# Optimization experiments

Hardware: AMD Instinct MI355X
Metric: run time of the kernel (lower is better)

The kernel has to match this reference:

```python
import jax, jax.numpy as jnp
import numpy as np

D_MODEL = 1024
NUM_HEADS = 16
NUM_KV_HEADS = 4
HEAD_DIM = D_MODEL // NUM_HEADS  # 64
THETA = 10000.0
MAX_SEQ_LEN = 4096


def _rope_tables(max_seq_len, d_k, theta):
    k_vec = jnp.arange(0, d_k, 2, dtype=jnp.float32) / d_k
    freq = 1.0 / (theta ** k_vec)                       # (d_k/2,)
    ang = jnp.arange(max_seq_len, dtype=jnp.float32)[:, None] * freq[None, :]
    return jnp.cos(ang), jnp.sin(ang)                   # each (max_seq_len, d_k/2)


def _apply_rope(x, pos, cos_table, sin_table):
    # x: (b, h, l, d), pos: (b, l)
    cos = cos_table[pos][:, None, :, :]                 # (b, 1, l, d/2)
    sin = sin_table[pos][:, None, :, :]
    even, odd = x[..., 0::2], x[..., 1::2]
    r1 = even * cos - odd * sin
    r2 = even * sin + odd * cos
    return jnp.stack([r1, r2], axis=-1).reshape(x.shape)  # interleave back


def setup_inputs() -> dict:
    key = jax.random.key(0)
    ks = jax.random.split(key, 6)
    B, L, D = 1, 4096, D_MODEL
    std = (2.0 / (D + D)) ** 0.5
    std_kv = (2.0 / (D + HEAD_DIM * NUM_KV_HEADS)) ** 0.5
    x = jax.random.normal(ks[0], (B, L, D), dtype=jnp.float32)
    Wq = jax.random.normal(ks[1], (D, D), dtype=jnp.float32) * std
    Wk = jax.random.normal(ks[2], (HEAD_DIM * NUM_KV_HEADS, D), dtype=jnp.float32) * std_kv
    Wv = jax.random.normal(ks[3], (HEAD_DIM * NUM_KV_HEADS, D), dtype=jnp.float32) * std_kv
    Wo = jax.random.normal(ks[4], (D, D), dtype=jnp.float32) * std
    token_positions = jnp.broadcast_to(jnp.arange(L, dtype=jnp.int32), (B, L))
    return {"x": x, "Wq": Wq, "Wk": Wk, "Wv": Wv, "Wo": Wo,
            "token_positions": token_positions}


def reference(x, Wq, Wk, Wv, Wo, token_positions):
    B, L, D = x.shape
    H, Hkv, Dh = NUM_HEADS, NUM_KV_HEADS, HEAD_DIM
    n_rep = H // Hkv
    cos_t, sin_t = _rope_tables(MAX_SEQ_LEN, Dh, THETA)

    q = (x @ Wq.T).reshape(B, L, H, Dh).transpose(0, 2, 1, 3)      # b h l d
    k = (x @ Wk.T).reshape(B, L, Hkv, Dh).transpose(0, 2, 1, 3)    # b g l d
    v = (x @ Wv.T).reshape(B, L, Hkv, Dh).transpose(0, 2, 1, 3)

    q = _apply_rope(q, token_positions, cos_t, sin_t)
    k = _apply_rope(k, token_positions, cos_t, sin_t)

    # GQA: group query heads by kv head
    qg = q.reshape(B, Hkv, n_rep, L, Dh)
    scores = jnp.einsum('bgrqd,bgkd->bgrqk', qg, k) / jnp.sqrt(jnp.float32(Dh))
    causal = jnp.tril(jnp.ones((L, L), dtype=bool))
    scores = jnp.where(causal, scores, -jnp.inf)
    weights = jax.nn.softmax(scores, axis=-1)
    out = jnp.einsum('bgrqk,bgkd->bgrqd', weights, v)              # b g r q d
    out = out.reshape(B, H, L, Dh).transpose(0, 2, 1, 3).reshape(B, L, D)
    return out @ Wo.T
```

## Files before the change

kernel.cpp:

```cpp
#include <hip/hip_runtime.h>
#include <hip/hip_bf16.h>
#include <math.h>

typedef __bf16 bf16;
typedef __bf16 v8bf __attribute__((ext_vector_type(8)));
typedef __bf16 v4bf __attribute__((ext_vector_type(4)));
typedef __bf16 v2bf __attribute__((ext_vector_type(2)));
typedef float f32x4 __attribute__((ext_vector_type(4)));
typedef float f32x16 __attribute__((ext_vector_type(16)));

#define L_SEQ 4096
#define DMODEL 1024
#define NHEADS 16
#define DH 64
#define NEG_BIG (-1e30f)
#define LN1E4_64 0.14391156f
#define SCL2 0.18033688f

static __device__ __forceinline__ unsigned pkbf(float x, float y) {
    v2bf t; t[0] = (bf16)x; t[1] = (bf16)y;
    return __builtin_bit_cast(unsigned, t);
}

__global__ void convert_all(const float* __restrict__ x, const float* __restrict__ wq,
                            const float* __restrict__ wk, const float* __restrict__ wv,
                            const float* __restrict__ wo,
                            bf16* __restrict__ xb, bf16* __restrict__ wqkvb,
                            bf16* __restrict__ wob) {
    int i = (blockIdx.x * 256 + threadIdx.x) * 4;
    const float* src;
    bf16* dst;
    if (i < 4194304)      { src = x  + i;             dst = xb    + i; }
    else if (i < 5242880) { src = wq + (i - 4194304); dst = wqkvb + (i - 4194304); }
    else if (i < 5505024) { src = wk + (i - 5242880); dst = wqkvb + 1048576 + (i - 5242880); }
    else if (i < 5767168) { src = wv + (i - 5505024); dst = wqkvb + 1310720 + (i - 5505024); }
    else                  { src = wo + (i - 5767168); dst = wob   + (i - 5767168); }
    f32x4 v = *(const f32x4*)src;
    v4bf r;
#pragma unroll
    for (int j = 0; j < 4; j++) r[j] = (bf16)v[j];
    *(v4bf*)dst = r;
}

__global__ __launch_bounds__(512) void gemm_qkv(const bf16* __restrict__ A,
                                                const bf16* __restrict__ W,
                                                bf16* __restrict__ Qb,
                                                bf16* __restrict__ Kb,
                                                bf16* __restrict__ Vtg,
                                                const int* __restrict__ tp) {
    __shared__ bf16 As[128][68];
    __shared__ bf16 Bs[128][68];
    const int K = 1024;
    const int tid = threadIdx.x;
    const int w = tid >> 6, lane = tid & 63;
    const int quad = lane >> 4, l16 = lane & 15;
    const int wm = (w & 1) * 64, wn = (w >> 1) * 32;
    const int bm = blockIdx.y * 128, bn = blockIdx.x * 128;

    f32x4 acc[4][2];
#pragma unroll
    for (int mf = 0; mf < 4; mf++)
#pragma unroll
        for (int nf = 0; nf < 2; nf++) acc[mf][nf] = (f32x4){0.f, 0.f, 0.f, 0.f};

    const int sr = tid >> 2;
    const int scb = (tid & 3) * 16;

    v8bf pa0, pa1, pb0, pb1;
    {
        const bf16* ap = &A[(size_t)(bm + sr) * K + scb];
        const bf16* bp = &W[(size_t)(bn + sr) * K + scb];
        pa0 = *(const v8bf*)ap; pa1 = *(const v8bf*)(ap + 8);
        pb0 = *(const v8bf*)bp; pb1 = *(const v8bf*)(bp + 8);
        *(v8bf*)&As[sr][scb] = pa0; *(v8bf*)&As[sr][scb + 8] = pa1;
        *(v8bf*)&Bs[sr][scb] = pb0; *(v8bf*)&Bs[sr][scb + 8] = pb1;
    }

    for (int kt = 0; kt < K; kt += 64) {
        __syncthreads();
        const bool more = (kt + 64) < K;
        if (more) {
            const bf16* ap = &A[(size_t)(bm + sr) * K + kt + 64 + scb];
            const bf16* bp = &W[(size_t)(bn + sr) * K + kt + 64 + scb];
            pa0 = *(const v8bf*)ap; pa1 = *(const v8bf*)(ap + 8);
            pb0 = *(const v8bf*)bp; pb1 = *(const v8bf*)(bp + 8);
        }
#pragma unroll
        for (int kf = 0; kf < 2; kf++) {
            v8bf a[4], b[2];
#pragma unroll
            for (int mf = 0; mf < 4; mf++) a[mf] = *(v8bf*)&As[wm + mf * 16 + l16][kf * 32 + quad * 8];
#pragma unroll
            for (int nf = 0; nf < 2; nf++) b[nf] = *(v8bf*)&Bs[wn + nf * 16 + l16][kf * 32 + quad * 8];
#pragma unroll
            for (int mf = 0; mf < 4; mf++)
#pragma unroll
                for (int nf = 0; nf < 2; nf++)
                    acc[mf][nf] = __builtin_amdgcn_mfma_f32_16x16x32_bf16(a[mf], b[nf], acc[mf][nf], 0, 0, 0);
        }
        __syncthreads();
        if (more) {
            *(v8bf*)&As[sr][scb] = pa0; *(v8bf*)&As[sr][scb + 8] = pa1;
            *(v8bf*)&Bs[sr][scb] = pb0; *(v8bf*)&Bs[sr][scb + 8] = pb1;
        }
    }

    if (bn < 1024) {
#pragma unroll
        for (int mf = 0; mf < 4; mf++) {
            int pos_[4];
#pragma unroll
            for (int r = 0; r < 4; r++) pos_[r] = tp[bm + wm + mf * 16 + quad * 4 + r];
#pragma unroll
            for (int nf = 0; nf < 2; nf++) {
                const int col = bn + wn + nf * 16 + l16;
                float fr = __expf(-(float)((col & 63) & ~1) * LN1E4_64);
#pragma unroll
                for (int r = 0; r < 4; r++) {
                    float v = acc[mf][nf][r];
                    float sn, cs;
                    __sincosf((float)pos_[r] * fr, &sn, &cs);
                    float p = __shfl_xor(v, 1);
                    float res = (l16 & 1) ? (p * sn + v * cs) : (v * cs - p * sn);
                    int row = bm + wm + mf * 16 + quad * 4 + r;
                    Qb[(size_t)row * DMODEL + col] = (bf16)res;
                }
            }
        }
    } else if (bn < 1280) {
#pragma unroll
        for (int mf = 0; mf < 4; mf++) {
            int pos_[4];
#pragma unroll
            for (int r = 0; r < 4; r++) pos_[r] = tp[bm + wm + mf * 16 + quad * 4 + r];
#pragma unroll
            for (int nf = 0; nf < 2; nf++) {
                const int kcol = bn - 1024 + wn + nf * 16 + l16;
                float fr = __expf(-(float)((kcol & 63) & ~1) * LN1E4_64);
#pragma unroll
                for (int r = 0; r < 4; r++) {
                    float v = acc[mf][nf][r];
                    float sn, cs;
                    __sincosf((float)pos_[r] * fr, &sn, &cs);
                    float p = __shfl_xor(v, 1);
                    float res = (l16 & 1) ? (p * sn + v * cs) : (v * cs - p * sn);
                    int row = bm + wm + mf * 16 + quad * 4 + r;
                    Kb[(size_t)row * 256 + kcol] = (bf16)res;
                }
            }
        }
    } else {
#pragma unroll
        for (int mf = 0; mf < 4; mf++)
#pragma unroll
            for (int nf = 0; nf < 2; nf++) {
                v4bf pk;
#pragma unroll
                for (int r = 0; r < 4; r++) pk[r] = (bf16)acc[mf][nf][r];
                int vcol = bn - 1280 + wn + nf * 16 + l16;
                int row = bm + wm + mf * 16 + quad * 4;
                *(v4bf*)&Vtg[(size_t)vcol * L_SEQ + row] = pk;
            }
    }
}

__global__ __launch_bounds__(512) void gemm_out(const bf16* __restrict__ A,
                                                const bf16* __restrict__ W,
                                                float* __restrict__ C) {
    __shared__ bf16 As[128][68];
    __shared__ bf16 Bs[128][68];
    const int K = 1024, N = 1024;
    const int tid = threadIdx.x;
    const int w = tid >> 6, lane = tid & 63;
    const int quad = lane >> 4, l16 = lane & 15;
    const int wm = (w & 1) * 64, wn = (w >> 1) * 32;
    const int bm = blockIdx.y * 128, bn = blockIdx.x * 128;

    f32x4 acc[4][2];
#pragma unroll
    for (int mf = 0; mf < 4; mf++)
#pragma unroll
        for (int nf = 0; nf < 2; nf++) acc[mf][nf] = (f32x4){0.f, 0.f, 0.f, 0.f};

    const int sr = tid >> 2;
    const int scb = (tid & 3) * 16;

    v8bf pa0, pa1, pb0, pb1;
    {
        const bf16* ap = &A[(size_t)(bm + sr) * K + scb];
        const bf16* bp = &W[(size_t)(bn + sr) * K + scb];
        pa0 = *(const v8bf*)ap; pa1 = *(const v8bf*)(ap + 8);
        pb0 = *(const v8bf*)bp; pb1 = *(const v8bf*)(bp + 8);
        *(v8bf*)&As[sr][scb] = pa0; *(v8bf*)&As[sr][scb + 8] = pa1;
        *(v8bf*)&Bs[sr][scb] = pb0; *(v8bf*)&Bs[sr][scb + 8] = pb1;
    }

    for (int kt = 0; kt < K; kt += 64) {
        __syncthreads();
        const bool more = (kt + 64) < K;
        if (more) {
            const bf16* ap = &A[(size_t)(bm + sr) * K + kt + 64 + scb];
            const bf16* bp = &W[(size_t)(bn + sr) * K + kt + 64 + scb];
            pa0 = *(const v8bf*)ap; pa1 = *(const v8bf*)(ap + 8);
            pb0 = *(const v8bf*)bp; pb1 = *(const v8bf*)(bp + 8);
        }
#pragma unroll
        for (int kf = 0; kf < 2; kf++) {
            v8bf a[4], b[2];
#pragma unroll
            for (int mf = 0; mf < 4; mf++) a[mf] = *(v8bf*)&As[wm + mf * 16 + l16][kf * 32 + quad * 8];
#pragma unroll
            for (int nf = 0; nf < 2; nf++) b[nf] = *(v8bf*)&Bs[wn + nf * 16 + l16][kf * 32 + quad * 8];
#pragma unroll
            for (int mf = 0; mf < 4; mf++)
#pragma unroll
                for (int nf = 0; nf < 2; nf++)
                    acc[mf][nf] = __builtin_amdgcn_mfma_f32_16x16x32_bf16(a[mf], b[nf], acc[mf][nf], 0, 0, 0);
        }
        __syncthreads();
        if (more) {
            *(v8bf*)&As[sr][scb] = pa0; *(v8bf*)&As[sr][scb + 8] = pa1;
            *(v8bf*)&Bs[sr][scb] = pb0; *(v8bf*)&Bs[sr][scb + 8] = pb1;
        }
    }
#pragma unroll
    for (int mf = 0; mf < 4; mf++)
#pragma unroll
        for (int nf = 0; nf < 2; nf++)
#pragma unroll
            for (int r = 0; r < 4; r++) {
                int row = bm + wm + mf * 16 + quad * 4 + r;
                int col = bn + wn + nf * 16 + l16;
                C[(size_t)row * N + col] = acc[mf][nf][r];
            }
}

__global__ __launch_bounds__(256, 2) void flash7(const bf16* __restrict__ Q,
                                                 const bf16* __restrict__ Kb,
                                                 const bf16* __restrict__ Vtg,
                                                 bf16* __restrict__ O0,
                                                 bf16* __restrict__ O1,
                                                 float* __restrict__ ML) {
    __shared__ bf16 Ks[128][68];
    __shared__ bf16 Vt[64][132];
    const int h = blockIdx.y, kvh = h >> 2;
    const int bx = blockIdx.x;
    const int tid = threadIdx.x;
    const int w = tid >> 6, lane = tid & 63;
    const int l32 = lane & 31, hi = lane >> 5;
    const int krow = tid >> 1, kcb = (tid & 1) * 32;
    const int vr = tid >> 2, vcb = (tid & 3) * 32;

    for (int p = 0; p < 2; p++) {
        const int qb = p ? (31 - bx) : bx;
        const int T = qb + 1;
        const int k0 = p ? ((T + 1) >> 1) : 0;
        const int k1 = p ? T : ((T + 1) >> 1);
        bf16* Op = p ? O1 : O0;
        float* mlp = ML + (size_t)(p * NHEADS + h) * L_SEQ * 2;

        if (k0 >= k1) {
            for (int i = tid; i < 128 * 64; i += 256) {
                int rr = i >> 6, cc = i & 63;
                Op[(size_t)(qb * 128 + rr) * DMODEL + h * DH + cc] = (bf16)0.f;
            }
            if (tid < 128) {
                mlp[(qb * 128 + tid) * 2 + 0] = NEG_BIG;
                mlp[(qb * 128 + tid) * 2 + 1] = 0.f;
            }
            continue;
        }

        const int qrow = qb * 128 + w * 32 + l32;
        v8bf qf[4];
#pragma unroll
        for (int d16 = 0; d16 < 4; d16++)
            qf[d16] = *(const v8bf*)&Q[(size_t)qrow * DMODEL + h * DH + d16 * 16 + hi * 8];

        f32x16 oaccT[2];
#pragma unroll
        for (int d = 0; d < 2; d++)
#pragma unroll
            for (int r = 0; r < 16; r++) oaccT[d][r] = 0.f;
        float m_i = NEG_BIG, l_i = 0.f;

        v8bf kreg[4], vreg[4];
        {
            const bf16* ks = &Kb[(size_t)(k0 * 128 + krow) * 256 + kvh * DH + kcb];
            const bf16* vs = &Vtg[(size_t)(kvh * DH + vr) * L_SEQ + k0 * 128 + vcb];
#pragma unroll
            for (int u = 0; u < 4; u++) { kreg[u] = *(const v8bf*)&ks[8 * u]; vreg[u] = *(const v8bf*)&vs[8 * u]; }
            __syncthreads();
#pragma unroll
            for (int u = 0; u < 4; u++) { *(v8bf*)&Ks[krow][kcb + 8 * u] = kreg[u]; *(v8bf*)&Vt[vr][vcb + 8 * u] = vreg[u]; }
        }

        for (int kb = k0; kb < k1; kb++) {
            __syncthreads();
            if (kb + 1 < k1) {
                const bf16* ks = &Kb[(size_t)((kb + 1) * 128 + krow) * 256 + kvh * DH + kcb];
                const bf16* vs = &Vtg[(size_t)(kvh * DH + vr) * L_SEQ + (kb + 1) * 128 + vcb];
#pragma unroll
                for (int u = 0; u < 4; u++) { kreg[u] = *(const v8bf*)&ks[8 * u]; vreg[u] = *(const v8bf*)&vs[8 * u]; }
            }

            f32x16 s[4];
            __builtin_amdgcn_s_setprio(1);
#pragma unroll
            for (int n = 0; n < 4; n++) {
#pragma unroll
                for (int r = 0; r < 16; r++) s[n][r] = 0.f;
#pragma unroll
                for (int d16 = 0; d16 < 4; d16++) {
                    v8bf av = *(v8bf*)&Ks[n * 32 + l32][d16 * 16 + hi * 8];
                    s[n] = __builtin_amdgcn_mfma_f32_32x32x16_bf16(av, qf[d16], s[n], 0, 0, 0);
                }
            }
            __builtin_amdgcn_s_setprio(0);

            if (kb == qb) {
#pragma unroll
                for (int n = 0; n < 4; n++) {
                    int kbase = kb * 128 + n * 32 + 4 * hi;
#pragma unroll
                    for (int r = 0; r < 16; r++) {
                        int key = kbase + (r & 3) + 8 * (r >> 2);
                        s[n][r] = (key <= qrow) ? s[n][r] * SCL2 : NEG_BIG;
                    }
                }
            } else {
#pragma unroll
                for (int n = 0; n < 4; n++)
#pragma unroll
                    for (int r = 0; r < 16; r++) s[n][r] *= SCL2;
            }

            float mx = s[0][0];
#pragma unroll
            for (int n = 0; n < 4; n++)
#pragma unroll
                for (int r = 0; r < 16; r++) mx = fmaxf(mx, s[n][r]);
            mx = fmaxf(mx, __shfl_xor(mx, 32));

            float mnew = fmaxf(m_i, mx);
            float alpha = exp2f(m_i - mnew);
            float rs = 0.f;
#pragma unroll
            for (int n = 0; n < 4; n++)
#pragma unroll
                for (int r = 0; r < 16; r++) {
                    float pv = exp2f(s[n][r] - mnew);
                    s[n][r] = pv;
                    rs += pv;
                }
            rs += __shfl_xor(rs, 32);
            l_i = l_i * alpha + rs;
            m_i = mnew;
#pragma unroll
            for (int d = 0; d < 2; d++)
#pragma unroll
                for (int r = 0; r < 16; r++) oaccT[d][r] *= alpha;

            __builtin_amdgcn_s_setprio(1);
#pragma unroll
            for (int n = 0; n < 4; n++) {
#pragma unroll
                for (int u = 0; u < 2; u++) {
                    const int ro = u * 8;
                    unsigned a0 = pkbf(s[n][ro + 0], s[n][ro + 1]);
                    unsigned a1 = pkbf(s[n][ro + 2], s[n][ro + 3]);
                    unsigned b0 = pkbf(s[n][ro + 4], s[n][ro + 5]);
                    unsigned b1 = pkbf(s[n][ro + 6], s[n][ro + 7]);
#if __has_builtin(__builtin_amdgcn_permlane32_swap)
                    auto s0 = __builtin_amdgcn_permlane32_swap(a0, b0, false, false);
                    auto s1 = __builtin_amdgcn_permlane32_swap(a1, b1, false, false);
                    unsigned w0 = s0[0], w2 = s0[1], w1 = s1[0], w3 = s1[1];
#else
                    unsigned t0 = hi ? a0 : b0;
                    unsigned r0 = __shfl_xor(t0, 32);
                    unsigned w0 = hi ? r0 : a0, w2 = hi ? b0 : r0;
                    unsigned t1 = hi ? a1 : b1;
                    unsigned r1 = __shfl_xor(t1, 32);
                    unsigned w1 = hi ? r1 : a1, w3 = hi ? b1 : r1;
#endif
                    union { unsigned uu[4]; v8bf v; } pf;
                    pf.uu[0] = w0; pf.uu[1] = w1; pf.uu[2] = w2; pf.uu[3] = w3;
                    const int t = n * 2 + u;
#pragma unroll
                    for (int dblk = 0; dblk < 2; dblk++) {
                        v8bf av = *(v8bf*)&Vt[dblk * 32 + l32][t * 16 + hi * 8];
                        oaccT[dblk] = __builtin_amdgcn_mfma_f32_32x32x16_bf16(av, pf.v, oaccT[dblk], 0, 0, 0);
                    }
                }
            }
            __builtin_amdgcn_s_setprio(0);

            __syncthreads();
            if (kb + 1 < k1) {
#pragma unroll
                for (int u = 0; u < 4; u++) { *(v8bf*)&Ks[krow][kcb + 8 * u] = kreg[u]; *(v8bf*)&Vt[vr][vcb + 8 * u] = vreg[u]; }
            }
        }

        __syncthreads();
#pragma unroll
        for (int dblk = 0; dblk < 2; dblk++)
#pragma unroll
            for (int r = 0; r < 16; r++) {
                int d = dblk * 32 + (r & 3) + 8 * (r >> 2) + 4 * hi;
                Ks[w * 32 + l32][d] = (bf16)oaccT[dblk][r];
            }
        asm volatile("s_waitcnt lgkmcnt(0)" ::: "memory");
        __builtin_amdgcn_sched_barrier(0);
#pragma unroll
        for (int i = 0; i < 4; i++) {
            int cc = (lane & 1) * 32 + i * 8;
            int rr = w * 32 + (lane >> 1);
            v8bf ov = *(v8bf*)&Ks[rr][cc];
            *(v8bf*)&Op[(size_t)(qb * 128 + rr) * DMODEL + h * DH + cc] = ov;
        }
        if (hi == 0) {
            mlp[qrow * 2 + 0] = m_i;
            mlp[qrow * 2 + 1] = l_i;
        }
    }
}

__global__ void combine(const bf16* __restrict__ O0, const bf16* __restrict__ O1,
                        const float* __restrict__ ML, bf16* __restrict__ Attn) {
    int gid = blockIdx.x * 256 + threadIdx.x;
    int row = gid >> 8;
    int cg = (gid & 255) * 4;
    int h = cg >> 6;
    const float* ml0 = ML + ((size_t)h * L_SEQ + row) * 2;
    const float* ml1 = ML + ((size_t)(NHEADS + h) * L_SEQ + row) * 2;
    float m0 = ml0[0], l0 = ml0[1], m1 = ml1[0], l1 = ml1[1];
    float m = fmaxf(m0, m1);
    float a0 = exp2f(m0 - m), a1 = exp2f(m1 - m);
    float inv = 1.f / (a0 * l0 + a1 * l1);
    v4bf o0 = *(const v4bf*)&O0[(size_t)row * DMODEL + cg];
    v4bf o1 = *(const v4bf*)&O1[(size_t)row * DMODEL + cg];
    v4bf res;
#pragma unroll
    for (int j = 0; j < 4; j++)
        res[j] = (bf16)((a0 * (float)o0[j] + a1 * (float)o1[j]) * inv);
    *(v4bf*)&Attn[(size_t)row * DMODEL + cg] = res;
}

extern "C" void kernel_launch(void* const* d_in, const int* in_sizes, int n_in,
                              void* d_out, int out_size, void* d_ws, size_t ws_size,
                              hipStream_t stream) {
    const float* x  = (const float*)d_in[0];
    const float* Wq = (const float*)d_in[1];
    const float* Wk = (const float*)d_in[2];
    const float* Wv = (const float*)d_in[3];
    const float* Wo = (const float*)d_in[4];
    const int*   tp = (const int*)d_in[5];
    float* out = (float*)d_out;

    bf16*  xb    = (bf16*)d_ws;
    bf16*  wqkvb = xb    + 4194304;
    bf16*  wob   = wqkvb + 1572864;
    bf16*  Qb    = wob   + 1048576;
    bf16*  Kb    = Qb    + 4194304;
    bf16*  Vtg   = Kb    + 1048576;
    float* MLf   = (float*)(Vtg + 1048576);
    bf16*  Attn  = xb;
    bf16*  O0    = (bf16*)d_out;
    bf16*  O1    = O0 + 4194304;

    convert_all<<<6656, 256, 0, stream>>>(x, Wq, Wk, Wv, Wo, xb, wqkvb, wob);
    gemm_qkv<<<dim3(12, 32), 512, 0, stream>>>(xb, wqkvb, Qb, Kb, Vtg, tp);
    flash7<<<dim3(32, NHEADS), 256, 0, stream>>>(Qb, Kb, Vtg, O0, O1, MLf);
    combine<<<4096, 256, 0, stream>>>(O0, O1, MLf, Attn);
    gemm_out<<<dim3(8, 32), 512, 0, stream>>>(Attn, wob, out);
}
```

Before: 206.3 us.

## Split flash attention halves across grid z, defer rescale, fold softmax scale into Q

The two key-range halves that each flash block used to process in a loop now run as separate blocks via a third grid dimension, with launch bounds raised to four blocks per CU and heaviest query blocks scheduled first. The softmax scale (including log2e) is folded into Q at the QKV GEMM epilogue, which removes the per-score multiply. The online-softmax rescale of the accumulator is skipped unless the running max grows by more than a threshold, and the max reduction is rewritten. The raised occupancy target may constrain registers, and deferred rescaling lets exponentials grow up to 2^8, which could affect bf16 accuracy of P.

```diff
diff --git a/kernel.cpp b/kernel.cpp
--- a/kernel.cpp
+++ b/kernel.cpp
@@ -16,6 +16,7 @@
 #define NEG_BIG (-1e30f)
 #define LN1E4_64 0.14391156f
 #define SCL2 0.18033688f
+#define DEFER_THR 8.0f
 
 static __device__ __forceinline__ unsigned pkbf(float x, float y) {
     v2bf t; t[0] = (bf16)x; t[1] = (bf16)y;
@@ -123,7 +124,7 @@
                     float p = __shfl_xor(v, 1);
                     float res = (l16 & 1) ? (p * sn + v * cs) : (v * cs - p * sn);
                     int row = bm + wm + mf * 16 + quad * 4 + r;
-                    Qb[(size_t)row * DMODEL + col] = (bf16)res;
+                    Qb[(size_t)row * DMODEL + col] = (bf16)(res * SCL2);
                 }
             }
         }
@@ -235,7 +236,7 @@
             }
 }
 
-__global__ __launch_bounds__(256, 2) void flash7(const bf16* __restrict__ Q,
+__global__ __launch_bounds__(256, 4) void flash8(const bf16* __restrict__ Q,
                                                  const bf16* __restrict__ Kb,
                                                  const bf16* __restrict__ Vtg,
                                                  bf16* __restrict__ O0,
@@ -244,185 +245,181 @@
     __shared__ bf16 Ks[128][68];
     __shared__ bf16 Vt[64][132];
     const int h = blockIdx.y, kvh = h >> 2;
-    const int bx = blockIdx.x;
+    const int z = blockIdx.z;
+    const int qb = 31 - blockIdx.x;
     const int tid = threadIdx.x;
     const int w = tid >> 6, lane = tid & 63;
     const int l32 = lane & 31, hi = lane >> 5;
     const int krow = tid >> 1, kcb = (tid & 1) * 32;
     const int vr = tid >> 2, vcb = (tid & 3) * 32;
 
-    for (int p = 0; p < 2; p++) {
-        const int qb = p ? (31 - bx) : bx;
-        const int T = qb + 1;
-        const int k0 = p ? ((T + 1) >> 1) : 0;
-        const int k1 = p ? T : ((T + 1) >> 1);
-        bf16* Op = p ? O1 : O0;
-        float* mlp = ML + (size_t)(p * NHEADS + h) * L_SEQ * 2;
-
-        if (k0 >= k1) {
-            for (int i = tid; i < 128 * 64; i += 256) {
-                int rr = i >> 6, cc = i & 63;
-                Op[(size_t)(qb * 128 + rr) * DMODEL + h * DH + cc] = (bf16)0.f;
-            }
-            if (tid < 128) {
-                mlp[(qb * 128 + tid) * 2 + 0] = NEG_BIG;
-                mlp[(qb * 128 + tid) * 2 + 1] = 0.f;
-            }
-            continue;
-        }
-
-        const int qrow = qb * 128 + w * 32 + l32;
-        v8bf qf[4];
-#pragma unroll
-        for (int d16 = 0; d16 < 4; d16++)
-            qf[d16] = *(const v8bf*)&Q[(size_t)qrow * DMODEL + h * DH + d16 * 16 + hi * 8];
-
-        f32x16 oaccT[2];
-#pragma unroll
-        for (int d = 0; d < 2; d++)
-#pragma unroll
-            for (int r = 0; r < 16; r++) oaccT[d][r] = 0.f;
-        float m_i = NEG_BIG, l_i = 0.f;
-
-        v8bf kreg[4], vreg[4];
-        {
-            const bf16* ks = &Kb[(size_t)(k0 * 128 + krow) * 256 + kvh * DH + kcb];
-            const bf16* vs = &Vtg[(size_t)(kvh * DH + vr) * L_SEQ + k0 * 128 + vcb];
+    const int T = qb + 1;
+    const int k0 = z ? ((T + 1) >> 1) : 0;
+    const int k1 = z ? T : ((T + 1) >> 1);
+    bf16* Op = z ? O1 : O0;
+    float* mlp = ML + (size_t)(z * NHEADS + h) * L_SEQ * 2;
+
+    if (k0 >= k1) {
+        for (int i = tid; i < 128 * 64; i += 256) {
+            int rr = i >> 6, cc = i & 63;
+            Op[(size_t)(qb * 128 + rr) * DMODEL + h * DH + cc] = (bf16)0.f;
+        }
+        if (tid < 128) {
+            mlp[(qb * 128 + tid) * 2 + 0] = NEG_BIG;
+            mlp[(qb * 128 + tid) * 2 + 1] = 0.f;
+        }
+        return;
+    }
+
+    const int qrow = qb * 128 + w * 32 + l32;
+    v8bf qf[4];
+#pragma unroll
+    for (int d16 = 0; d16 < 4; d16++)
+        qf[d16] = *(const v8bf*)&Q[(size_t)qrow * DMODEL + h * DH + d16 * 16 + hi * 8];
+
+    f32x16 oaccT[2];
+#pragma unroll
+    for (int d = 0; d < 2; d++)
+#pragma unroll
+        for (int r = 0; r < 16; r++) oaccT[d][r] = 0.f;
+    float m_i = NEG_BIG, l_i = 0.f;
+
+    v8bf kreg[4], vreg[4];
+    {
+        const bf16* ks = &Kb[(size_t)(k0 * 128 + krow) * 256 + kvh * DH + kcb];
+        const bf16* vs = &Vtg[(size_t)(kvh * DH + vr) * L_SEQ + k0 * 128 + vcb];
+#pragma unroll
+        for (int u = 0; u < 4; u++) { kreg[u] = *(const v8bf*)&ks[8 * u]; vreg[u] = *(const v8bf*)&vs[8 * u]; }
+#pragma unroll
+        for (int u = 0; u < 4; u++) { *(v8bf*)&Ks[krow][kcb + 8 * u] = kreg[u]; *(v8bf*)&Vt[vr][vcb + 8 * u] = vreg[u]; }
+    }
+
+    for (int kb = k0; kb < k1; kb++) {
+        __syncthreads();
+        if (kb + 1 < k1) {
+            const bf16* ks = &Kb[(size_t)((kb + 1) * 128 + krow) * 256 + kvh * DH + kcb];
+            const bf16* vs = &Vtg[(size_t)(kvh * DH + vr) * L_SEQ + (kb + 1) * 128 + vcb];
 #pragma unroll
             for (int u = 0; u < 4; u++) { kreg[u] = *(const v8bf*)&ks[8 * u]; vreg[u] = *(const v8bf*)&vs[8 * u]; }
-            __syncthreads();
-#pragma unroll
-            for (int u = 0; u < 4; u++) { *(v8bf*)&Ks[krow][kcb + 8 * u] = kreg[u]; *(v8bf*)&Vt[vr][vcb + 8 * u] = vreg[u]; }
-        }
-
-        for (int kb = k0; kb < k1; kb++) {
-            __syncthreads();
-            if (kb + 1 < k1) {
-                const bf16* ks = &Kb[(size_t)((kb + 1) * 128 + krow) * 256 + kvh * DH + kcb];
-                const bf16* vs = &Vtg[(size_t)(kvh * DH + vr) * L_SEQ + (kb + 1) * 128 + vcb];
-#pragma unroll
-                for (int u = 0; u < 4; u++) { kreg[u] = *(const v8bf*)&ks[8 * u]; vreg[u] = *(const v8bf*)&vs[8 * u]; }
-            }
-
-            f32x16 s[4];
-            __builtin_amdgcn_s_setprio(1);
+        }
+
+        f32x16 s[4];
+        __builtin_amdgcn_s_setprio(1);
+#pragma unroll
+        for (int n = 0; n < 4; n++) {
+#pragma unroll
+            for (int r = 0; r < 16; r++) s[n][r] = 0.f;
+#pragma unroll
+            for (int d16 = 0; d16 < 4; d16++) {
+                v8bf av = *(v8bf*)&Ks[n * 32 + l32][d16 * 16 + hi * 8];
+                s[n] = __builtin_amdgcn_mfma_f32_32x32x16_bf16(av, qf[d16], s[n], 0, 0, 0);
+            }
+        }
+        __builtin_amdgcn_s_setprio(0);
+
+        if (kb == qb) {
 #pragma unroll
             for (int n = 0; n < 4; n++) {
-#pragma unroll
-                for (int r = 0; r < 16; r++) s[n][r] = 0.f;
-#pragma unroll
-                for (int d16 = 0; d16 < 4; d16++) {
-                    v8bf av = *(v8bf*)&Ks[n * 32 + l32][d16 * 16 + hi * 8];
-                    s[n] = __builtin_amdgcn_mfma_f32_32x32x16_bf16(av, qf[d16], s[n], 0, 0, 0);
+                int kbase = kb * 128 + n * 32 + 4 * hi;
+#pragma unroll
+                for (int r = 0; r < 16; r++) {
+                    int key = kbase + (r & 3) + 8 * (r >> 2);
+                    if (key > qrow) s[n][r] = NEG_BIG;
                 }
             }
-            __builtin_amdgcn_s_setprio(0);
-
-            if (kb == qb) {
-#pragma unroll
-                for (int n = 0; n < 4; n++) {
-                    int kbase = kb * 128 + n * 32 + 4 * hi;
-#pragma unroll
-                    for (int r = 0; r < 16; r++) {
-                        int key = kbase + (r & 3) + 8 * (r >> 2);
-                        s[n][r] = (key <= qrow) ? s[n][r] * SCL2 : NEG_BIG;
-                    }
-                }
-            } else {
-#pragma unroll
-                for (int n = 0; n < 4; n++)
-#pragma unroll
-                    for (int r = 0; r < 16; r++) s[n][r] *= SCL2;
-            }
-
-            float mx = s[0][0];
-#pragma unroll
-            for (int n = 0; n < 4; n++)
-#pragma unroll
-                for (int r = 0; r < 16; r++) mx = fmaxf(mx, s[n][r]);
-            mx = fmaxf(mx, __shfl_xor(mx, 32));
-
+        }
+
+        float mx = NEG_BIG;
+#pragma unroll
+        for (int n = 0; n < 4; n++)
+#pragma unroll
+            for (int r = 0; r < 16; r += 2)
+                mx = fmaxf(fmaxf(mx, s[n][r]), s[n][r + 1]);
+        mx = fmaxf(mx, __shfl_xor(mx, 32));
+
+        if (!__all(mx <= m_i + DEFER_THR)) {
             float mnew = fmaxf(m_i, mx);
             float alpha = exp2f(m_i - mnew);
-            float rs = 0.f;
-#pragma unroll
-            for (int n = 0; n < 4; n++)
-#pragma unroll
-                for (int r = 0; r < 16; r++) {
-                    float pv = exp2f(s[n][r] - mnew);
-                    s[n][r] = pv;
-                    rs += pv;
+            l_i *= alpha;
+#pragma unroll
+            for (int d = 0; d < 2; d++)
+#pragma unroll
+                for (int r = 0; r < 16; r++) oaccT[d][r] *= alpha;
+            m_i = mnew;
+        }
+
+        float rs = 0.f;
+#pragma unroll
+        for (int n = 0; n < 4; n++)
+#pragma unroll
+            for (int r = 0; r < 16; r++) {
+                float pv = exp2f(s[n][r] - m_i);
+                s[n][r] = pv;
+                rs += pv;
+            }
+        rs += __shfl_xor(rs, 32);
+        l_i += rs;
+
+        __builtin_amdgcn_s_setprio(1);
+#pragma unroll
+        for (int n = 0; n < 4; n++) {
+#pragma unroll
+            for (int u = 0; u < 2; u++) {
+                const int ro = u * 8;
+                unsigned a0 = pkbf(s[n][ro + 0], s[n][ro + 1]);
+                unsigned a1 = pkbf(s[n][ro + 2], s[n][ro + 3]);
+                unsigned b0 = pkbf(s[n][ro + 4], s[n][ro + 5]);
+                unsigned b1 = pkbf(s[n][ro + 6], s[n][ro + 7]);
+#if __has_builtin(__builtin_amdgcn_permlane32_swap)
+                auto s0 = __builtin_amdgcn_permlane32_swap(a0, b0, false, false);
+                auto s1 = __builtin_amdgcn_permlane32_swap(a1, b1, false, false);
+                unsigned w0 = s0[0], w2 = s0[1], w1 = s1[0], w3 = s1[1];
+#else
+                unsigned t0 = hi ? a0 : b0;
+                unsigned r0 = __shfl_xor(t0, 32);
+                unsigned w0 = hi ? r0 : a0, w2 = hi ? b0 : r0;
+                unsigned t1 = hi ? a1 : b1;
+                unsigned r1 = __shfl_xor(t1, 32);
+                unsigned w1 = hi ? r1 : a1, w3 = hi ? b1 : r1;
+#endif
+                union { unsigned uu[4]; v8bf v; } pf;
+                pf.uu[0] = w0; pf.uu[1] = w1; pf.uu[2] = w2; pf.uu[3] = w3;
+                const int t = n * 2 + u;
+#pragma unroll
+                for (int dblk = 0; dblk < 2; dblk++) {
+                    v8bf av = *(v8bf*)&Vt[dblk * 32 + l32][t * 16 + hi * 8];
+                    oaccT[dblk] = __builtin_amdgcn_mfma_f32_32x32x16_bf16(av, pf.v, oaccT[dblk], 0, 0, 0);
                 }
-            rs += __shfl_xor(rs, 32);
-            l_i = l_i * alpha + rs;
-            m_i = mnew;
-#pragma unroll
-            for (int d = 0; d < 2; d++)
-#pragma unroll
-                for (int r = 0; r < 16; r++) oaccT[d][r] *= alpha;
-
-            __builtin_amdgcn_s_setprio(1);
-#pragma unroll
-            for (int n = 0; n < 4; n++) {
-#pragma unroll
-                for (int u = 0; u < 2; u++) {
-                    const int ro = u * 8;
-                    unsigned a0 = pkbf(s[n][ro + 0], s[n][ro + 1]);
-                    unsigned a1 = pkbf(s[n][ro + 2], s[n][ro + 3]);
-                    unsigned b0 = pkbf(s[n][ro + 4], s[n][ro + 5]);
-                    unsigned b1 = pkbf(s[n][ro + 6], s[n][ro + 7]);
-#if __has_builtin(__builtin_amdgcn_permlane32_swap)
-                    auto s0 = __builtin_amdgcn_permlane32_swap(a0, b0, false, false);
-                    auto s1 = __builtin_amdgcn_permlane32_swap(a1, b1, false, false);
-                    unsigned w0 = s0[0], w2 = s0[1], w1 = s1[0], w3 = s1[1];
-#else
-                    unsigned t0 = hi ? a0 : b0;
-                    unsigned r0 = __shfl_xor(t0, 32);
-                    unsigned w0 = hi ? r0 : a0, w2 = hi ? b0 : r0;
-                    unsigned t1 = hi ? a1 : b1;
-                    unsigned r1 = __shfl_xor(t1, 32);
-                    unsigned w1 = hi ? r1 : a1, w3 = hi ? b1 : r1;
-#endif
-                    union { unsigned uu[4]; v8bf v; } pf;
-                    pf.uu[0] = w0; pf.uu[1] = w1; pf.uu[2] = w2; pf.uu[3] = w3;
-                    const int t = n * 2 + u;
-#pragma unroll
-                    for (int dblk = 0; dblk < 2; dblk++) {
-                        v8bf av = *(v8bf*)&Vt[dblk * 32 + l32][t * 16 + hi * 8];
-                        oaccT[dblk] = __builtin_amdgcn_mfma_f32_32x32x16_bf16(av, pf.v, oaccT[dblk], 0, 0, 0);
-                    }
-                }
-            }
-            __builtin_amdgcn_s_setprio(0);
-
-            __syncthreads();
-            if (kb + 1 < k1) {
-#pragma unroll
-                for (int u = 0; u < 4; u++) { *(v8bf*)&Ks[krow][kcb + 8 * u] = kreg[u]; *(v8bf*)&Vt[vr][vcb + 8 * u] = vreg[u]; }
-            }
-        }
-
-        __syncthreads();
-#pragma unroll
-        for (int dblk = 0; dblk < 2; dblk++)
-#pragma unroll
-            for (int r = 0; r < 16; r++) {
-                int d = dblk * 32 + (r & 3) + 8 * (r >> 2) + 4 * hi;
-                Ks[w * 32 + l32][d] = (bf16)oaccT[dblk][r];
-            }
-        asm volatile("s_waitcnt lgkmcnt(0)" ::: "memory");
-        __builtin_amdgcn_sched_barrier(0);
-#pragma unroll
-        for (int i = 0; i < 4; i++) {
-            int cc = (lane & 1) * 32 + i * 8;
-            int rr = w * 32 + (lane >> 1);
-            v8bf ov = *(v8bf*)&Ks[rr][cc];
-            *(v8bf*)&Op[(size_t)(qb * 128 + rr) * DMODEL + h * DH + cc] = ov;
-        }
-        if (hi == 0) {
-            mlp[qrow * 2 + 0] = m_i;
-            mlp[qrow * 2 + 1] = l_i;
-        }
+            }
+        }
+        __builtin_amdgcn_s_setprio(0);
+
+        __syncthreads();
+        if (kb + 1 < k1) {
+#pragma unroll
+            for (int u = 0; u < 4; u++) { *(v8bf*)&Ks[krow][kcb + 8 * u] = kreg[u]; *(v8bf*)&Vt[vr][vcb + 8 * u] = vreg[u]; }
+        }
+    }
+
+#pragma unroll
+    for (int dblk = 0; dblk < 2; dblk++)
+#pragma unroll
+        for (int r = 0; r < 16; r++) {
+            int d = dblk * 32 + (r & 3) + 8 * (r >> 2) + 4 * hi;
+            Ks[w * 32 + l32][d] = (bf16)oaccT[dblk][r];
+        }
+    asm volatile("s_waitcnt lgkmcnt(0)" ::: "memory");
+    __builtin_amdgcn_sched_barrier(0);
+#pragma unroll
+    for (int i = 0; i < 4; i++) {
+        int cc = (lane & 1) * 32 + i * 8;
+        int rr = w * 32 + (lane >> 1);
+        v8bf ov = *(v8bf*)&Ks[rr][cc];
+        *(v8bf*)&Op[(size_t)(qb * 128 + rr) * DMODEL + h * DH + cc] = ov;
+    }
+    if (hi == 0) {
+        mlp[qrow * 2 + 0] = m_i;
+        mlp[qrow * 2 + 1] = l_i;
     }
 }
 
@@ -471,7 +468,7 @@
 
     convert_all<<<6656, 256, 0, stream>>>(x, Wq, Wk, Wv, Wo, xb, wqkvb, wob);
     gemm_qkv<<<dim3(12, 32), 512, 0, stream>>>(xb, wqkvb, Qb, Kb, Vtg, tp);
-    flash7<<<dim3(32, NHEADS), 256, 0, stream>>>(Qb, Kb, Vtg, O0, O1, MLf);
+    flash8<<<dim3(32, NHEADS, 2), 256, 0, stream>>>(Qb, Kb, Vtg, O0, O1, MLf);
     combine<<<4096, 256, 0, stream>>>(O0, O1, MLf, Attn);
     gemm_out<<<dim3(8, 32), 512, 0, stream>>>(Attn, wob, out);
 }
```

Result: slower. 313.6 us (+52.0%).
